# Kernel optimization log

Measured on AMD Instinct MI355X. Metric: run time of the kernel, lower is better.

The kernel has to match this reference:

```python
import jax, jax.numpy as jnp
import numpy as np

NEG_SLOPE = 0.2
EPS = 1e-16


def gat_conv(x, src, dst, W, att_src, att_dst, bias, heads, out_ch):
    """PyG-style GATConv. src/dst already include self-loops. Messages flow src -> dst."""
    N = x.shape[0]
    h = (x @ W).reshape(N, heads, out_ch)          # [N, H, C]
    a_src = jnp.sum(h * att_src, axis=-1)          # [N, H]
    a_dst = jnp.sum(h * att_dst, axis=-1)          # [N, H]
    e = a_src[src] + a_dst[dst]                    # [E, H]
    e = jax.nn.leaky_relu(e, NEG_SLOPE)
    # softmax over incoming edges per destination node
    m = jax.ops.segment_max(e, dst, num_segments=N)      # [N, H]
    m = jnp.where(jnp.isfinite(m), m, 0.0)
    ex = jnp.exp(e - m[dst])                       # [E, H]
    denom = jax.ops.segment_sum(ex, dst, num_segments=N)  # [N, H]
    alpha = ex / (denom[dst] + EPS)                # [E, H]
    msg = alpha[:, :, None] * h[src]               # [E, H, C]
    out = jax.ops.segment_sum(msg, dst, num_segments=N)   # [N, H, C]
    return out, bias


def add_self_loops(edge_index, N):
    loop = jnp.arange(N, dtype=edge_index.dtype)
    src = jnp.concatenate([edge_index[0], loop])
    dst = jnp.concatenate([edge_index[1], loop])
    return src, dst


def setup_inputs() -> dict:
    key = jax.random.key(0)
    ks = jax.random.split(key, 10)
    N, E, IN, HID, OUT, H = 100000, 1600000, 128, 32, 32, 4
    s = lambda fan: 1.0 / np.sqrt(fan)
    return {
        "x": jax.random.normal(ks[0], (N, IN), dtype=jnp.float32),
        "edge_index": jax.random.randint(ks[1], (2, E), 0, N, dtype=jnp.int32),
        "W1": jax.random.normal(ks[2], (IN, H * HID), dtype=jnp.float32) * s(IN),
        "att_src1": jax.random.normal(ks[3], (H, HID), dtype=jnp.float32) * s(HID),
        "att_dst1": jax.random.normal(ks[4], (H, HID), dtype=jnp.float32) * s(HID),
        "b1": jnp.zeros((H * HID,), dtype=jnp.float32),
        "W2": jax.random.normal(ks[5], (H * HID, OUT), dtype=jnp.float32) * s(H * HID),
        "att_src2": jax.random.normal(ks[6], (1, OUT), dtype=jnp.float32) * s(OUT),
        "att_dst2": jax.random.normal(ks[7], (1, OUT), dtype=jnp.float32) * s(OUT),
        "b2": jnp.zeros((OUT,), dtype=jnp.float32),
    }


def reference(x, edge_index, W1, att_src1, att_dst1, b1, W2, att_src2, att_dst2, b2):
    N = x.shape[0]
    src, dst = add_self_loops(edge_index, N)
    # layer 1: 4 heads, concat=True
    out1, bias1 = gat_conv(x, src, dst, W1, att_src1, att_dst1, b1, heads=4, out_ch=32)
    h1 = jax.nn.relu(out1.reshape(N, -1) + bias1)          # [N, 128]
    # layer 2: 1 head, concat=False (mean over 1 head == squeeze)
    out2, bias2 = gat_conv(h1, src, dst, W2, att_src2, att_dst2, b2, heads=1, out_ch=32)
    return out2.mean(axis=1) + bias2                       # [N, 32]
```

## Files before the change

### kernel.cpp

```cpp
#include <hip/hip_runtime.h>
#include <hip/hip_bf16.h>


typedef __bf16 bf16x8 __attribute__((ext_vector_type(8)));
typedef float f32x4 __attribute__((ext_vector_type(4)));

__device__ __forceinline__ float lrelu(float v) { return v >= 0.f ? v : 0.2f * v; }

__device__ __forceinline__ unsigned f2bf(float f) {
    unsigned u = __float_as_uint(f);
    return (u + 0x7FFFu + ((u >> 16) & 1u)) >> 16;
}

__device__ __forceinline__ bf16x8 as_bf16x8(uint4 u) {
    union { uint4 u; bf16x8 b; } c; c.u = u; return c.b;
}

__device__ __forceinline__ void bf16x8_fma(uint4 hv, float a, float* acc) {
    acc[0] = fmaf(a, __uint_as_float(hv.x << 16), acc[0]);
    acc[1] = fmaf(a, __uint_as_float(hv.x & 0xFFFF0000u), acc[1]);
    acc[2] = fmaf(a, __uint_as_float(hv.y << 16), acc[2]);
    acc[3] = fmaf(a, __uint_as_float(hv.y & 0xFFFF0000u), acc[3]);
    acc[4] = fmaf(a, __uint_as_float(hv.z << 16), acc[4]);
    acc[5] = fmaf(a, __uint_as_float(hv.z & 0xFFFF0000u), acc[5]);
    acc[6] = fmaf(a, __uint_as_float(hv.w << 16), acc[6]);
    acc[7] = fmaf(a, __uint_as_float(hv.w & 0xFFFF0000u), acc[7]);
}

__global__ __launch_bounds__(256) void cast_w_k(const float* __restrict__ W1,
                                                const float* __restrict__ W2,
                                                ushort* __restrict__ w1t,
                                                ushort* __restrict__ w2t) {
    int tid = blockIdx.x * 256 + threadIdx.x;
    if (tid < 16384) {
        int k = tid >> 7, c = tid & 127;
        w1t[c * 128 + k] = (ushort)f2bf(W1[tid]);
    }
    if (tid < 4096) {
        int k = tid >> 5, c = tid & 31;
        w2t[c * 128 + k] = (ushort)f2bf(W2[tid]);
    }
}

__global__ __launch_bounds__(256) void gemm1_hist_k(
    const float* __restrict__ x, const ushort* __restrict__ w1t,
    const float* __restrict__ atts, const float* __restrict__ attd,
    ushort* __restrict__ h, float* __restrict__ as_, float* __restrict__ ad_,
    const int* __restrict__ ei, int* __restrict__ deg, ushort* __restrict__ rank,
    int N, int E, int nbG, int nbE8) {
    const int g = blockIdx.x / 3;
    const int r = blockIdx.x % 3;

    if (r == 2) {
        if (g >= nbE8) return;
        const int base = (g * 256 + threadIdx.x) * 8;
        if (base >= E) return;
        int dd[8];
        if (base + 8 <= E) {
            int4 a = *(const int4*)&ei[E + base];
            int4 c = *(const int4*)&ei[E + base + 4];
            dd[0] = a.x; dd[1] = a.y; dd[2] = a.z; dd[3] = a.w;
            dd[4] = c.x; dd[5] = c.y; dd[6] = c.z; dd[7] = c.w;
        } else {
#pragma unroll
            for (int k = 0; k < 8; k++) {
                int e = base + k;
                dd[k] = (e < E) ? ei[E + e] : 0;
            }
        }
        int rr[8];
#pragma unroll
        for (int k = 0; k < 8; k++) {
            int e = base + k;
            if (e < E) rr[k] = atomicAdd(&deg[dd[k]], 1);
        }
        if (base + 8 <= E) {
            uint4 pk;
            pk.x = (unsigned)(rr[0] & 0xFFFF) | ((unsigned)(rr[1] & 0xFFFF) << 16);
            pk.y = (unsigned)(rr[2] & 0xFFFF) | ((unsigned)(rr[3] & 0xFFFF) << 16);
            pk.z = (unsigned)(rr[4] & 0xFFFF) | ((unsigned)(rr[5] & 0xFFFF) << 16);
            pk.w = (unsigned)(rr[6] & 0xFFFF) | ((unsigned)(rr[7] & 0xFFFF) << 16);
            *(uint4*)&rank[base] = pk;
        } else {
#pragma unroll
            for (int k = 0; k < 8; k++) if (base + k < E) rank[base + k] = (ushort)rr[k];
        }
        return;
    }

    const int gb = g * 2 + r;
    if (gb >= nbG) return;
    const int w = threadIdx.x >> 6;
    const int l = threadIdx.x & 63;
    const int c15 = l & 15;
    const int quad = l >> 4;
    const int n_base = gb * 64 + w * 16;
    const int n = n_base + c15;

    bf16x8 a[4];
    if (n < N) {
        const float4* xr = (const float4*)(x + (size_t)n * 128);
#pragma unroll
        for (int ks = 0; ks < 4; ks++) {
            float4 p0 = xr[ks * 8 + quad * 2];
            float4 p1 = xr[ks * 8 + quad * 2 + 1];
            uint4 u;
            u.x = f2bf(p0.x) | (f2bf(p0.y) << 16);
            u.y = f2bf(p0.z) | (f2bf(p0.w) << 16);
            u.z = f2bf(p1.x) | (f2bf(p1.y) << 16);
            u.w = f2bf(p1.z) | (f2bf(p1.w) << 16);
            a[ks] = as_bf16x8(u);
        }
    } else {
        uint4 z = make_uint4(0, 0, 0, 0);
#pragma unroll
        for (int ks = 0; ks < 4; ks++) a[ks] = as_bf16x8(z);
    }

    f32x4 acc[8];
#pragma unroll
    for (int ct = 0; ct < 8; ct++) acc[ct] = (f32x4){0.f, 0.f, 0.f, 0.f};

#pragma unroll
    for (int ct = 0; ct < 8; ct++) {
        const uint4* wr = (const uint4*)(w1t + (size_t)(ct * 16 + c15) * 128);
#pragma unroll
        for (int ks = 0; ks < 4; ks++) {
            bf16x8 bfrag = as_bf16x8(wr[ks * 4 + quad]);
            acc[ct] = __builtin_amdgcn_mfma_f32_16x16x32_bf16(a[ks], bfrag, acc[ct], 0, 0, 0);
        }
    }

#pragma unroll
    for (int ct = 0; ct < 8; ct++) {
        int col = ct * 16 + c15;
#pragma unroll
        for (int reg = 0; reg < 4; reg++) {
            int n_out = n_base + quad * 4 + reg;
            if (n_out < N) h[(size_t)n_out * 128 + col] = (ushort)f2bf(acc[ct][reg]);
        }
    }
#pragma unroll
    for (int hh = 0; hh < 4; hh++) {
        float sA = atts[hh * 32 + c15], sB = atts[hh * 32 + 16 + c15];
        float dA = attd[hh * 32 + c15], dB = attd[hh * 32 + 16 + c15];
#pragma unroll
        for (int reg = 0; reg < 4; reg++) {
            float ps = acc[2 * hh][reg] * sA + acc[2 * hh + 1][reg] * sB;
            float pd = acc[2 * hh][reg] * dA + acc[2 * hh + 1][reg] * dB;
            ps += __shfl_xor(ps, 1); pd += __shfl_xor(pd, 1);
            ps += __shfl_xor(ps, 2); pd += __shfl_xor(pd, 2);
            ps += __shfl_xor(ps, 4); pd += __shfl_xor(pd, 4);
            ps += __shfl_xor(ps, 8); pd += __shfl_xor(pd, 8);
            int n_out = n_base + quad * 4 + reg;
            if (c15 == 0 && n_out < N) { as_[n_out * 4 + hh] = ps; ad_[n_out * 4 + hh] = pd; }
        }
    }
}

__global__ __launch_bounds__(256) void scan1_k(const int* __restrict__ deg,
                                               int* __restrict__ tmp, int* __restrict__ partial, int N) {
    __shared__ int sh[256];
    int i = blockIdx.x * 256 + threadIdx.x;
    int v = (i < N) ? deg[i] + 1 : 0;
    sh[threadIdx.x] = v;
    __syncthreads();
#pragma unroll
    for (int off = 1; off < 256; off <<= 1) {
        int t = (threadIdx.x >= off) ? sh[threadIdx.x - off] : 0;
        __syncthreads();
        sh[threadIdx.x] += t;
        __syncthreads();
    }
    if (i < N) tmp[i] = sh[threadIdx.x];
    if (threadIdx.x == 255) partial[blockIdx.x] = sh[255];
}

__global__ __launch_bounds__(1024) void scan2_k(int* __restrict__ partial, int B) {
    __shared__ int sh[1024];
    int i = threadIdx.x;
    int v = (i < B) ? partial[i] : 0;
    sh[i] = v;
    __syncthreads();
#pragma unroll
    for (int off = 1; off < 1024; off <<= 1) {
        int t = (i >= off) ? sh[i - off] : 0;
        __syncthreads();
        sh[i] += t;
        __syncthreads();
    }
    if (i < B) partial[i] = sh[i] - v;
}

__global__ __launch_bounds__(256) void scan3_k(const int* __restrict__ tmp, const int* __restrict__ partial,
                                               const int* __restrict__ deg,
                                               int* __restrict__ rs, int* __restrict__ csr, int N) {
    int i = blockIdx.x * 256 + threadIdx.x;
    if (i < N) {
        int inc = tmp[i] + partial[blockIdx.x];
        rs[i + 1] = inc;
        csr[inc - deg[i] - 1] = i;
    }
    if (i == 0) rs[0] = 0;
}

__global__ __launch_bounds__(256) void scatter_k(const int* __restrict__ ei, const ushort* __restrict__ rank,
                                                 const int* __restrict__ rs, int E,
                                                 int* __restrict__ csr) {
    const int base = (blockIdx.x * 256 + threadIdx.x) * 4;
    if (base >= E) return;
#pragma unroll
    for (int k = 0; k < 4; k++) {
        int e = base + k;
        if (e < E) {
            int s = ei[e], d = ei[E + e];
            csr[rs[d] + 1 + (int)rank[e]] = s;
        }
    }
}

__global__ __launch_bounds__(256) void gather1_k(
    const int* __restrict__ rs, const int* __restrict__ csr,
    const float* __restrict__ as_, const float* __restrict__ ad_,
    const uint4* __restrict__ h, const float* __restrict__ b,
    const ushort* __restrict__ w2t, const float* __restrict__ atts2,
    const float* __restrict__ attd2,
    ushort* __restrict__ h2, float* __restrict__ as2, float* __restrict__ ad2,
    int N) {
    __shared__ uint4 o1s[16][18];
    const int jj = threadIdx.x & 31;
    const int l16 = jj & 15;
    const int sub = jj & 16;
    const int dl = (threadIdx.x >> 5) * 2 + (jj >> 4);
    const int d = blockIdx.x * 16 + dl;
    const int hl = l16 >> 2;
    const int sl = l16 & 3;
    int beg = 0, end = 0;
    float adv = 0.f;
    if (d < N) { beg = rs[d]; end = rs[d + 1]; adv = ad_[d * 4 + hl]; }

    float acc[8];
#pragma unroll
    for (int i = 0; i < 8; i++) acc[i] = 0.f;
    float den = 0.f;

    int j0 = beg;
    int sv0 = 0, sv1 = 0;
    float ex0 = 0.f, ex1 = 0.f;
    bool have = (j0 + 8 <= end);
    if (have) {
        sv0 = csr[j0 + sl];
        sv1 = csr[j0 + sl + 4];
        ex0 = __expf(fminf(lrelu(as_[sv0 * 4 + hl] + adv), 80.f));
        ex1 = __expf(fminf(lrelu(as_[sv1 * 4 + hl] + adv), 80.f));
    }
    while (have) {
        bool nhave = (j0 + 16 <= end);
        int na = nhave ? (j0 + 8) : beg;
        int psv0 = csr[na + sl];
        int psv1 = csr[na + sl + 4];
        den += ex0 + ex1;
        float av[8]; uint4 hv[8];
#pragma unroll
        for (int e = 0; e < 8; e++) {
            const int k = e >> 2, q = e & 3;
            const int srcl = sub + (l16 & 12) + q;
            float exk = k ? ex1 : ex0;
            int   svk = k ? sv1 : sv0;
            av[e] = __shfl(exk, srcl, 32);
            int s = __shfl(svk, srcl, 32);
            hv[e] = h[(size_t)s * 16 + l16];
        }
        float pex0 = __expf(fminf(lrelu(as_[psv0 * 4 + hl] + adv), 80.f));
        float pex1 = __expf(fminf(lrelu(as_[psv1 * 4 + hl] + adv), 80.f));
#pragma unroll
        for (int e = 0; e < 8; e++) bf16x8_fma(hv[e], av[e], acc);
        sv0 = psv0; sv1 = psv1; ex0 = pex0; ex1 = pex1;
        j0 += 8; have = nhave;
    }
    int r = end - j0;
    if (r > 0) {
        float ex0r = 0.f, ex1r = 0.f;
        int   sv0r = 0,   sv1r = 0;
        if (sl < r) {
            sv0r = csr[j0 + sl];
            ex0r = __expf(fminf(lrelu(as_[sv0r * 4 + hl] + adv), 80.f));
            den += ex0r;
        }
        if (sl + 4 < r) {
            sv1r = csr[j0 + sl + 4];
            ex1r = __expf(fminf(lrelu(as_[sv1r * 4 + hl] + adv), 80.f));
            den += ex1r;
        }
        float av[8]; uint4 hv[8];
#pragma unroll
        for (int e = 0; e < 8; e++) {
            const int k = e >> 2, q = e & 3;
            const int srcl = sub + (l16 & 12) + q;
            float exk = k ? ex1r : ex0r;
            int   svk = k ? sv1r : sv0r;
            av[e] = __shfl(exk, srcl, 32);
            int s = __shfl(svk, srcl, 32);
            if (e < r) hv[e] = h[(size_t)s * 16 + l16];
        }
#pragma unroll
        for (int e = 0; e < 8; e++) if (e < r) bf16x8_fma(hv[e], av[e], acc);
    }
    den += __shfl_xor(den, 1, 32);
    den += __shfl_xor(den, 2, 32);
    const float rcp = 1.f / (den + 1e-16f);
    float4 b0 = *(const float4*)&b[l16 * 8];
    float4 b1 = *(const float4*)&b[l16 * 8 + 4];
    float v0 = fmaxf(acc[0] * rcp + b0.x, 0.f);
    float v1 = fmaxf(acc[1] * rcp + b0.y, 0.f);
    float v2 = fmaxf(acc[2] * rcp + b0.z, 0.f);
    float v3 = fmaxf(acc[3] * rcp + b0.w, 0.f);
    float v4 = fmaxf(acc[4] * rcp + b1.x, 0.f);
    float v5 = fmaxf(acc[5] * rcp + b1.y, 0.f);
    float v6 = fmaxf(acc[6] * rcp + b1.z, 0.f);
    float v7 = fmaxf(acc[7] * rcp + b1.w, 0.f);
    uint4 pk;
    pk.x = f2bf(v0) | (f2bf(v1) << 16);
    pk.y = f2bf(v2) | (f2bf(v3) << 16);
    pk.z = f2bf(v4) | (f2bf(v5) << 16);
    pk.w = f2bf(v6) | (f2bf(v7) << 16);
    o1s[dl][l16] = pk;
    __syncthreads();

    if (threadIdx.x < 64) {
        const int l = threadIdx.x;
        const int c15g = l & 15;
        const int quad = l >> 4;
        bf16x8 a2[4];
#pragma unroll
        for (int ks = 0; ks < 4; ks++) a2[ks] = as_bf16x8(o1s[c15g][ks * 4 + quad]);
        f32x4 acc2[2];
#pragma unroll
        for (int ct = 0; ct < 2; ct++) acc2[ct] = (f32x4){0.f, 0.f, 0.f, 0.f};
#pragma unroll
        for (int ct = 0; ct < 2; ct++) {
            const uint4* wr = (const uint4*)(w2t + (size_t)(ct * 16 + c15g) * 128);
#pragma unroll
            for (int ks = 0; ks < 4; ks++) {
                bf16x8 bfrag = as_bf16x8(wr[ks * 4 + quad]);
                acc2[ct] = __builtin_amdgcn_mfma_f32_16x16x32_bf16(a2[ks], bfrag, acc2[ct], 0, 0, 0);
            }
        }
        const int nb = blockIdx.x * 16;
#pragma unroll
        for (int ct = 0; ct < 2; ct++) {
            int col = ct * 16 + c15g;
#pragma unroll
            for (int reg = 0; reg < 4; reg++) {
                int n_out = nb + quad * 4 + reg;
                if (n_out < N) h2[(size_t)n_out * 32 + col] = (ushort)f2bf(acc2[ct][reg]);
            }
        }
        float sA = atts2[c15g], sB = atts2[16 + c15g];
        float dA = attd2[c15g], dB = attd2[16 + c15g];
#pragma unroll
        for (int reg = 0; reg < 4; reg++) {
            float ps = acc2[0][reg] * sA + acc2[1][reg] * sB;
            float pd = acc2[0][reg] * dA + acc2[1][reg] * dB;
            ps += __shfl_xor(ps, 1); pd += __shfl_xor(pd, 1);
            ps += __shfl_xor(ps, 2); pd += __shfl_xor(pd, 2);
            ps += __shfl_xor(ps, 4); pd += __shfl_xor(pd, 4);
            ps += __shfl_xor(ps, 8); pd += __shfl_xor(pd, 8);
            int n_out = nb + quad * 4 + reg;
            if (c15g == 0 && n_out < N) { as2[n_out] = ps; ad2[n_out] = pd; }
        }
    }
}

__global__ __launch_bounds__(256) void gather2_k(
    const int* __restrict__ rs, const int* __restrict__ csr,
    const float* __restrict__ as_, const float* __restrict__ ad_,
    const uint4* __restrict__ h, const float* __restrict__ b,
    float* __restrict__ o, int N) {
    const int jj = threadIdx.x & 31;
    const int l4 = jj & 3;
    const int sub = jj & 28;
    const int d = blockIdx.x * 64 + (threadIdx.x >> 5) * 8 + (jj >> 2);
    if (d >= N) return;
    const int beg = rs[d], end = rs[d + 1];
    const float adv = ad_[d];

    float acc[8];
#pragma unroll
    for (int i = 0; i < 8; i++) acc[i] = 0.f;
    float den = 0.f;

    int j0 = beg;
    int sv0 = 0, sv1 = 0;
    float ex0 = 0.f, ex1 = 0.f;
    bool have = (j0 + 8 <= end);
    if (have) {
        sv0 = csr[j0 + l4];
        sv1 = csr[j0 + l4 + 4];
        ex0 = __expf(fminf(lrelu(as_[sv0] + adv), 80.f));
        ex1 = __expf(fminf(lrelu(as_[sv1] + adv), 80.f));
    }
    while (have) {
        bool nhave = (j0 + 16 <= end);
        int na = nhave ? (j0 + 8) : beg;
        int psv0 = csr[na + l4];
        int psv1 = csr[na + l4 + 4];
        den += ex0 + ex1;
        float av[8]; uint4 hv[8];
#pragma unroll
        for (int e = 0; e < 8; e++) {
            const int k = e >> 2, q = e & 3;
            const int srcl = sub + q;
            float exk = k ? ex1 : ex0;
            int   svk = k ? sv1 : sv0;
            av[e] = __shfl(exk, srcl, 32);
            int s = __shfl(svk, srcl, 32);
            hv[e] = h[(size_t)s * 4 + l4];
        }
        float pex0 = __expf(fminf(lrelu(as_[psv0] + adv), 80.f));
        float pex1 = __expf(fminf(lrelu(as_[psv1] + adv), 80.f));
#pragma unroll
        for (int e = 0; e < 8; e++) bf16x8_fma(hv[e], av[e], acc);
        sv0 = psv0; sv1 = psv1; ex0 = pex0; ex1 = pex1;
        j0 += 8; have = nhave;
    }
    int r = end - j0;
    if (r > 0) {
        float ex0r = 0.f, ex1r = 0.f;
        int   sv0r = 0,   sv1r = 0;
        if (l4 < r) {
            sv0r = csr[j0 + l4];
            ex0r = __expf(fminf(lrelu(as_[sv0r] + adv), 80.f));
            den += ex0r;
        }
        if (l4 + 4 < r) {
            sv1r = csr[j0 + l4 + 4];
            ex1r = __expf(fminf(lrelu(as_[sv1r] + adv), 80.f));
            den += ex1r;
        }
        float av[8]; uint4 hv[8];
#pragma unroll
        for (int e = 0; e < 8; e++) {
            const int k = e >> 2, q = e & 3;
            const int srcl = sub + q;
            float exk = k ? ex1r : ex0r;
            int   svk = k ? sv1r : sv0r;
            av[e] = __shfl(exk, srcl, 32);
            int s = __shfl(svk, srcl, 32);
            if (e < r) hv[e] = h[(size_t)s * 4 + l4];
        }
#pragma unroll
        for (int e = 0; e < 8; e++) if (e < r) bf16x8_fma(hv[e], av[e], acc);
    }
    den += __shfl_xor(den, 1, 32);
    den += __shfl_xor(den, 2, 32);
    const float rcp = 1.f / (den + 1e-16f);
    float4 b0 = *(const float4*)&b[l4 * 8];
    float4 b1 = *(const float4*)&b[l4 * 8 + 4];
    float4 o0, o1v;
    o0.x  = acc[0] * rcp + b0.x;
    o0.y  = acc[1] * rcp + b0.y;
    o0.z  = acc[2] * rcp + b0.z;
    o0.w  = acc[3] * rcp + b0.w;
    o1v.x = acc[4] * rcp + b1.x;
    o1v.y = acc[5] * rcp + b1.y;
    o1v.z = acc[6] * rcp + b1.z;
    o1v.w = acc[7] * rcp + b1.w;
    *(float4*)&o[(size_t)d * 32 + l4 * 8]     = o0;
    *(float4*)&o[(size_t)d * 32 + l4 * 8 + 4] = o1v;
}

extern "C" void kernel_launch(void* const* d_in, const int* in_sizes, int n_in,
                              void* d_out, int out_size, void* d_ws, size_t ws_size,
                              hipStream_t stream) {
    const float* x    = (const float*)d_in[0];
    const int*   ei   = (const int*)d_in[1];
    const float* W1   = (const float*)d_in[2];
    const float* as1v = (const float*)d_in[3];
    const float* ad1v = (const float*)d_in[4];
    const float* b1   = (const float*)d_in[5];
    const float* W2   = (const float*)d_in[6];
    const float* as2v = (const float*)d_in[7];
    const float* ad2v = (const float*)d_in[8];
    const float* b2   = (const float*)d_in[9];
    float* out = (float*)d_out;

    const int N = in_sizes[0] / 128;
    const int E = in_sizes[1] / 2;
    const int EN = E + N;
    const int B = (N + 255) / 256;

    char* base = (char*)d_ws;
    size_t o = 0;
    auto alloc = [&](size_t bytes) { void* p = base + o; o += (bytes + 255) & ~(size_t)255; return p; };
    ushort* w1t  = (ushort*)alloc((size_t)128 * 128 * 2);
    ushort* w2t  = (ushort*)alloc((size_t)32 * 128 * 2);
    ushort* h1   = (ushort*)alloc((size_t)N * 128 * 2);
    ushort* h2   = (ushort*)alloc((size_t)N * 32 * 2);
    float*  as1  = (float*)alloc((size_t)N * 4 * 4);
    float*  ad1  = (float*)alloc((size_t)N * 4 * 4);
    float*  as2  = (float*)alloc((size_t)N * 4);
    float*  ad2  = (float*)alloc((size_t)N * 4);
    int*    deg  = (int*)alloc((size_t)N * 4);
    int*    tmp  = (int*)alloc((size_t)N * 4);
    int*    part = (int*)alloc((size_t)1024 * 4);
    int*    rs   = (int*)alloc((size_t)(N + 1) * 4);
    ushort* rank = (ushort*)alloc((size_t)E * 2);
    int*    csr  = (int*)alloc((size_t)EN * 4);

    hipMemsetAsync(deg, 0, (size_t)N * 4, stream);

    const int nbE8 = ((E + 7) / 8 + 255) / 256;
    const int nbE4 = ((E + 3) / 4 + 255) / 256;
    const int nbN = (N + 255) / 256;
    const int nbG = (N + 63) / 64;

    const int ngrp = max((nbG + 1) / 2, nbE8);

    cast_w_k<<<64, 256, 0, stream>>>(W1, W2, w1t, w2t);
    gemm1_hist_k<<<ngrp * 3, 256, 0, stream>>>(x, w1t, as1v, ad1v, h1, as1, ad1,
                                               ei, deg, rank, N, E, nbG, nbE8);
    scan1_k<<<nbN, 256, 0, stream>>>(deg, tmp, part, N);
    scan2_k<<<1, 1024, 0, stream>>>(part, B);
    scan3_k<<<nbN, 256, 0, stream>>>(tmp, part, deg, rs, csr, N);
    scatter_k<<<nbE4, 256, 0, stream>>>(ei, rank, rs, E, csr);

    gather1_k<<<(N + 15) / 16, 256, 0, stream>>>(rs, csr, as1, ad1, (const uint4*)h1, b1,
                                                 w2t, as2v, ad2v, h2, as2, ad2, N);

    gather2_k<<<(N + 63) / 64, 256, 0, stream>>>(rs, csr, as2, ad2, (const uint4*)h2, b2, out, N);
}
```

Measured before the change: 325.5 us.

## Replace three-kernel prefix scan with single-pass decoupled look-back scan

The three scan kernels (block scan, partial scan, apply) are merged into one kernel that uses a dynamic block ticket and decoupled look-back over per-block status words to get each block's prefix. The hipMemsetAsync of the degree array and the new partial/ticket initialisation move into the weight-cast kernel. This removes two kernel launches, one memset, and the round trip of the tmp array through memory. In exchange, the look-back is a serial spin by one thread per block on predecessor flags, and correctness depends on atomic visibility between blocks.

```diff
diff --git a/kernel.cpp b/kernel.cpp
--- a/kernel.cpp
+++ b/kernel.cpp
@@ -30,7 +30,11 @@
 __global__ __launch_bounds__(256) void cast_w_k(const float* __restrict__ W1,
                                                 const float* __restrict__ W2,
                                                 ushort* __restrict__ w1t,
-                                                ushort* __restrict__ w2t) {
+                                                ushort* __restrict__ w2t,
+                                                int* __restrict__ deg,
+                                                unsigned long long* __restrict__ part,
+                                                int* __restrict__ ticket,
+                                                int N, int nblk) {
     int tid = blockIdx.x * 256 + threadIdx.x;
     if (tid < 16384) {
         int k = tid >> 7, c = tid & 127;
@@ -40,6 +44,9 @@
         int k = tid >> 5, c = tid & 31;
         w2t[c * 128 + k] = (ushort)f2bf(W2[tid]);
     }
+    for (int i = tid; i < N; i += 64 * 256) deg[i] = 0;
+    if (tid < nblk) part[tid] = 0ULL;
+    if (tid == 0) *ticket = 0;
 }
 
 __global__ __launch_bounds__(256) void gemm1_hist_k(
@@ -158,12 +165,17 @@
     }
 }
 
-__global__ __launch_bounds__(256) void scan1_k(const int* __restrict__ deg,
-                                               int* __restrict__ tmp, int* __restrict__ partial, int N) {
+__global__ __launch_bounds__(256) void scan_k(
+    const int* __restrict__ deg, int* __restrict__ rs, int* __restrict__ csr,
+    unsigned long long* __restrict__ part, int* __restrict__ ticket, int N) {
     __shared__ int sh[256];
-    int i = blockIdx.x * 256 + threadIdx.x;
-    int v = (i < N) ? deg[i] + 1 : 0;
-    sh[threadIdx.x] = v;
+    __shared__ int bid_s, pfx_s;
+    if (threadIdx.x == 0) bid_s = atomicAdd(ticket, 1);
+    __syncthreads();
+    const int bid = bid_s;
+    const int i = bid * 256 + threadIdx.x;
+    const int dv = (i < N) ? deg[i] + 1 : 0;
+    sh[threadIdx.x] = dv;
     __syncthreads();
 #pragma unroll
     for (int off = 1; off < 256; off <<= 1) {
@@ -172,34 +184,26 @@
         sh[threadIdx.x] += t;
         __syncthreads();
     }
-    if (i < N) tmp[i] = sh[threadIdx.x];
-    if (threadIdx.x == 255) partial[blockIdx.x] = sh[255];
-}
-
-__global__ __launch_bounds__(1024) void scan2_k(int* __restrict__ partial, int B) {
-    __shared__ int sh[1024];
-    int i = threadIdx.x;
-    int v = (i < B) ? partial[i] : 0;
-    sh[i] = v;
+    const int total = sh[255];
+    if (threadIdx.x == 0) {
+        atomicExch(&part[bid], (1ULL << 32) | (unsigned)total);
+        int running = 0;
+        int j = bid - 1;
+        while (j >= 0) {
+            unsigned long long wrd = atomicAdd(&part[j], 0ULL);
+            unsigned st = (unsigned)(wrd >> 32);
+            if (st == 2u)      { running += (int)(unsigned)wrd; break; }
+            else if (st == 1u) { running += (int)(unsigned)wrd; j--; }
+        }
+        pfx_s = running;
+        atomicExch(&part[bid], (2ULL << 32) | (unsigned)(running + total));
+    }
     __syncthreads();
-#pragma unroll
-    for (int off = 1; off < 1024; off <<= 1) {
-        int t = (i >= off) ? sh[i - off] : 0;
-        __syncthreads();
-        sh[i] += t;
-        __syncthreads();
-    }
-    if (i < B) partial[i] = sh[i] - v;
-}
-
-__global__ __launch_bounds__(256) void scan3_k(const int* __restrict__ tmp, const int* __restrict__ partial,
-                                               const int* __restrict__ deg,
-                                               int* __restrict__ rs, int* __restrict__ csr, int N) {
-    int i = blockIdx.x * 256 + threadIdx.x;
+    const int pfx = pfx_s;
     if (i < N) {
-        int inc = tmp[i] + partial[blockIdx.x];
+        int inc = pfx + sh[threadIdx.x];
         rs[i + 1] = inc;
-        csr[inc - deg[i] - 1] = i;
+        csr[inc - dv] = i;
     }
     if (i == 0) rs[0] = 0;
 }
@@ -488,7 +492,7 @@
     const int N = in_sizes[0] / 128;
     const int E = in_sizes[1] / 2;
     const int EN = E + N;
-    const int B = (N + 255) / 256;
+    const int nbN = (N + 255) / 256;
 
     char* base = (char*)d_ws;
     size_t o = 0;
@@ -502,27 +506,22 @@
     float*  as2  = (float*)alloc((size_t)N * 4);
     float*  ad2  = (float*)alloc((size_t)N * 4);
     int*    deg  = (int*)alloc((size_t)N * 4);
-    int*    tmp  = (int*)alloc((size_t)N * 4);
-    int*    part = (int*)alloc((size_t)1024 * 4);
+    unsigned long long* part = (unsigned long long*)alloc((size_t)(nbN + 1) * 8);
+    int*    tick = (int*)alloc((size_t)256);
     int*    rs   = (int*)alloc((size_t)(N + 1) * 4);
     ushort* rank = (ushort*)alloc((size_t)E * 2);
     int*    csr  = (int*)alloc((size_t)EN * 4);
 
-    hipMemsetAsync(deg, 0, (size_t)N * 4, stream);
-
     const int nbE8 = ((E + 7) / 8 + 255) / 256;
     const int nbE4 = ((E + 3) / 4 + 255) / 256;
-    const int nbN = (N + 255) / 256;
     const int nbG = (N + 63) / 64;
 
     const int ngrp = max((nbG + 1) / 2, nbE8);
 
-    cast_w_k<<<64, 256, 0, stream>>>(W1, W2, w1t, w2t);
+    cast_w_k<<<64, 256, 0, stream>>>(W1, W2, w1t, w2t, deg, part, tick, N, nbN);
     gemm1_hist_k<<<ngrp * 3, 256, 0, stream>>>(x, w1t, as1v, ad1v, h1, as1, ad1,
                                                ei, deg, rank, N, E, nbG, nbE8);
-    scan1_k<<<nbN, 256, 0, stream>>>(deg, tmp, part, N);
-    scan2_k<<<1, 1024, 0, stream>>>(part, B);
-    scan3_k<<<nbN, 256, 0, stream>>>(tmp, part, deg, rs, csr, N);
+    scan_k<<<nbN, 256, 0, stream>>>(deg, rs, csr, part, tick, N);
     scatter_k<<<nbE4, 256, 0, stream>>>(ei, rank, rs, E, csr);
 
     gather1_k<<<(N + 15) / 16, 256, 0, stream>>>(rs, csr, as1, ad1, (const uint4*)h1, b1,
```

Measured after the change: 332.0 us. 2.0% more time.
